# Kernel optimization log

Hardware: AMD Instinct MI355X
Metric: run time of the kernel (lower is better)

## Reference

```python
import math
import jax, jax.numpy as jnp
import numpy as np

ALL_OFFSETS = (1, 2, 3, 4, 5, 6, 7, 8, 9, 11, 13, 15, 16, 23, 32, 64, 128, 256, 512, 1024)
J = len(ALL_OFFSETS)

B, H, N, HD = 2, 16, 8192, 128


def setup_inputs() -> dict:
    key = jax.random.key(0)
    kq, kk, kv, kb, ks = jax.random.split(key, 5)
    return {
        "q": jax.random.normal(kq, (B, H, N, HD), dtype=jnp.float32),
        "k": jax.random.normal(kk, (B, H, N, HD), dtype=jnp.float32),
        "v": jax.random.normal(kv, (B, H, N, HD), dtype=jnp.float32),
        "pos_bias": jax.random.normal(kb, (J, H), dtype=jnp.float32),
        "scale_embed": jax.random.normal(ks, (J, HD), dtype=jnp.float32),
    }


def _dsqg_forward(q, k, v, pos_bias, scale_embed):
    # q,k,v: [B,H,N,HD]; pos_bias: [J,H]; scale_embed: [J,HD]
    b, h, n, hd = q.shape
    sc = 1.0 / math.sqrt(hd)
    idx = jnp.arange(n)
    qf = q.astype(jnp.float32)
    kf = k.astype(jnp.float32)
    vf = v.astype(jnp.float32)
    # learned scale-embedding term fused into scores: (q . se_j) * sc -> [B,H,N,J]
    qse = jnp.einsum('bhnd,jd->bhnj', qf, scale_embed.astype(jnp.float32)) * sc
    pb = pos_bias.astype(jnp.float32)  # [J,H]
    scores = []
    for j, delta in enumerate(ALL_OFFSETS):
        kp = idx - delta
        valid = kp >= 0
        kpc = jnp.clip(kp, 0)
        # gathered-key dot product: one key per query per offset
        s = jnp.einsum('bhnd,bhnd->bhn', qf, kf[:, :, kpc]) * sc
        s = s + pb[j][None, :, None] + qse[..., j]
        s = jnp.where(valid[None, None, :], s, -jnp.inf)
        scores.append(s)
    scores = jnp.stack(scores, axis=-1)  # [B,H,N,J]
    # stable softmax over the J offsets; rows with no valid offset produce 0 output
    m = jnp.max(scores, axis=-1, keepdims=True)
    m_safe = jnp.where(jnp.isfinite(m), m, 0.0)
    e = jnp.where(jnp.isfinite(scores), jnp.exp(scores - m_safe), 0.0)
    l = jnp.sum(e, axis=-1, keepdims=True)
    p = e / jnp.where(l > 0.0, l, 1.0)  # [B,H,N,J]
    out = jnp.zeros_like(qf)
    for j, delta in enumerate(ALL_OFFSETS):
        kpc = jnp.clip(idx - delta, 0)
        out = out + p[..., j:j + 1] * vf[:, :, kpc]
    return out.astype(q.dtype)


def reference(q, k, v, pos_bias, scale_embed):
    return _dsqg_forward(q, k, v, pos_bias, scale_embed)
```

## Files before the change

### kernel.cpp

```cpp
#include <hip/hip_runtime.h>
#include <math.h>

namespace {

constexpr int kB = 2, kH = 16, kN = 8192, kHD = 128, kJ = 20;
constexpr int kTQ = 64;
constexpr float kScale = 0.08838834764831845f;

__global__ __launch_bounds__(256, 4)
void dsqg_fwd(const float* __restrict__ q, const float* __restrict__ k,
              const float* __restrict__ v, const float* __restrict__ pb,
              const float* __restrict__ se, float* __restrict__ out) {
  constexpr int OFFS[kJ] = {1, 2, 3, 4, 5, 6, 7, 8, 9, 11,
                            13, 15, 16, 23, 32, 64, 128, 256, 512, 1024};
  __shared__ float s_se[kJ * kHD];
  __shared__ float s_pb[kJ];

  const int t = threadIdx.x;
  const int bh = blockIdx.y;
  const int h = bh & (kH - 1);
  const int n = blockIdx.x * kTQ + (t >> 2);
  const int part = t & 3;

  for (int i = t; i < kJ * kHD; i += 256) s_se[i] = se[i];
  if (t < kJ) s_pb[t] = pb[t * kH + h];
  __syncthreads();

  const size_t base = (size_t)bh * kN * kHD;
  const float4* qrow = (const float4*)(q + base + (size_t)n * kHD);
  float4 rq[8];
#pragma unroll
  for (int i = 0; i < 8; ++i) rq[i] = qrow[i * 4 + part];

  float sc[kJ];
#pragma unroll
  for (int j = 0; j < kJ; ++j) {
    const int delta = OFFS[j];
    int kr = n - delta;
    kr = kr < 0 ? 0 : kr;
    const float4* krow = (const float4*)(k + base + (size_t)kr * kHD);
    const float4* srow = (const float4*)(s_se + j * kHD);
    float acc = 0.f;
#pragma unroll
    for (int i = 0; i < 8; ++i) {
      float4 kv = krow[i * 4 + part];
      float4 sv = srow[i * 4 + part];
      acc += rq[i].x * (kv.x + sv.x);
      acc += rq[i].y * (kv.y + sv.y);
      acc += rq[i].z * (kv.z + sv.z);
      acc += rq[i].w * (kv.w + sv.w);
    }
    acc += __shfl_xor(acc, 1);
    acc += __shfl_xor(acc, 2);
    const float sj = acc * kScale + s_pb[j];
    sc[j] = (n >= delta) ? sj : -INFINITY;
  }

  float m = -INFINITY;
#pragma unroll
  for (int j = 0; j < kJ; ++j) m = fmaxf(m, sc[j]);
  const float msafe = (m == -INFINITY) ? 0.f : m;
  float l = 0.f;
#pragma unroll
  for (int j = 0; j < kJ; ++j) {
    const float e = (sc[j] == -INFINITY) ? 0.f : __expf(sc[j] - msafe);
    sc[j] = e;
    l += e;
  }
  const float inv = (l > 0.f) ? 1.f / l : 0.f;

  float4 o[8];
#pragma unroll
  for (int i = 0; i < 8; ++i) o[i] = make_float4(0.f, 0.f, 0.f, 0.f);
#pragma unroll
  for (int j = 0; j < kJ; ++j) {
    const float pj = sc[j] * inv;
    int vr = n - OFFS[j];
    vr = vr < 0 ? 0 : vr;
    const float4* vrow = (const float4*)(v + base + (size_t)vr * kHD);
#pragma unroll
    for (int i = 0; i < 8; ++i) {
      float4 vv = vrow[i * 4 + part];
      o[i].x += pj * vv.x;
      o[i].y += pj * vv.y;
      o[i].z += pj * vv.z;
      o[i].w += pj * vv.w;
    }
  }
  float4* orow = (float4*)(out + base + (size_t)n * kHD);
#pragma unroll
  for (int i = 0; i < 8; ++i) orow[i * 4 + part] = o[i];
}

}

extern "C" void kernel_launch(void* const* d_in, const int* in_sizes, int n_in,
                              void* d_out, int out_size, void* d_ws, size_t ws_size,
                              hipStream_t stream) {
  const float* q = (const float*)d_in[0];
  const float* k = (const float*)d_in[1];
  const float* v = (const float*)d_in[2];
  const float* pb = (const float*)d_in[3];
  const float* se = (const float*)d_in[4];
  float* out = (float*)d_out;

  dim3 grid(kN / kTQ, kB * kH);
  dsqg_fwd<<<grid, 256, 0, stream>>>(q, k, v, pb, se, out);
}
```

Before: 760.4 us.

## Swizzle workgroups across XCDs, use nontemporal q/out access, raise occupancy hint

```diff
diff --git a/kernel.cpp b/kernel.cpp
--- a/kernel.cpp
+++ b/kernel.cpp
@@ -5,9 +5,15 @@
 
 constexpr int kB = 2, kH = 16, kN = 8192, kHD = 128, kJ = 20;
 constexpr int kTQ = 64;
+constexpr int kNT = kN / kTQ;
+constexpr int kNWG = kB * kH * kNT;
+constexpr int kNXCD = 8;
+constexpr int kChunk = kNWG / kNXCD;
 constexpr float kScale = 0.08838834764831845f;
 
-__global__ __launch_bounds__(256, 4)
+typedef float f4 __attribute__((ext_vector_type(4)));
+
+__global__ __launch_bounds__(256, 8)
 void dsqg_fwd(const float* __restrict__ q, const float* __restrict__ k,
               const float* __restrict__ v, const float* __restrict__ pb,
               const float* __restrict__ se, float* __restrict__ out) {
@@ -17,9 +23,12 @@
   __shared__ float s_pb[kJ];
 
   const int t = threadIdx.x;
-  const int bh = blockIdx.y;
+  const int lin = blockIdx.x;
+  const int swz = (lin & (kNXCD - 1)) * kChunk + (lin >> 3);
+  const int bh = swz >> 7;
+  const int ntile = swz & (kNT - 1);
   const int h = bh & (kH - 1);
-  const int n = blockIdx.x * kTQ + (t >> 2);
+  const int n = ntile * kTQ + (t >> 2);
   const int part = t & 3;
 
   for (int i = t; i < kJ * kHD; i += 256) s_se[i] = se[i];
@@ -27,10 +36,10 @@
   __syncthreads();
 
   const size_t base = (size_t)bh * kN * kHD;
-  const float4* qrow = (const float4*)(q + base + (size_t)n * kHD);
-  float4 rq[8];
+  const f4* qrow = (const f4*)(q + base + (size_t)n * kHD);
+  f4 rq[8];
 #pragma unroll
-  for (int i = 0; i < 8; ++i) rq[i] = qrow[i * 4 + part];
+  for (int i = 0; i < 8; ++i) rq[i] = __builtin_nontemporal_load(&qrow[i * 4 + part]);
 
   float sc[kJ];
 #pragma unroll
@@ -38,13 +47,13 @@
     const int delta = OFFS[j];
     int kr = n - delta;
     kr = kr < 0 ? 0 : kr;
-    const float4* krow = (const float4*)(k + base + (size_t)kr * kHD);
-    const float4* srow = (const float4*)(s_se + j * kHD);
+    const f4* krow = (const f4*)(k + base + (size_t)kr * kHD);
+    const f4* srow = (const f4*)(s_se + j * kHD);
     float acc = 0.f;
 #pragma unroll
     for (int i = 0; i < 8; ++i) {
-      float4 kv = krow[i * 4 + part];
-      float4 sv = srow[i * 4 + part];
+      f4 kv = krow[i * 4 + part];
+      f4 sv = srow[i * 4 + part];
       acc += rq[i].x * (kv.x + sv.x);
       acc += rq[i].y * (kv.y + sv.y);
       acc += rq[i].z * (kv.z + sv.z);
@@ -69,27 +78,24 @@
   }
   const float inv = (l > 0.f) ? 1.f / l : 0.f;
 
-  float4 o[8];
+  f4 o[8];
 #pragma unroll
-  for (int i = 0; i < 8; ++i) o[i] = make_float4(0.f, 0.f, 0.f, 0.f);
+  for (int i = 0; i < 8; ++i) o[i] = (f4)(0.f);
 #pragma unroll
   for (int j = 0; j < kJ; ++j) {
     const float pj = sc[j] * inv;
     int vr = n - OFFS[j];
     vr = vr < 0 ? 0 : vr;
-    const float4* vrow = (const float4*)(v + base + (size_t)vr * kHD);
+    const f4* vrow = (const f4*)(v + base + (size_t)vr * kHD);
 #pragma unroll
     for (int i = 0; i < 8; ++i) {
-      float4 vv = vrow[i * 4 + part];
-      o[i].x += pj * vv.x;
-      o[i].y += pj * vv.y;
-      o[i].z += pj * vv.z;
-      o[i].w += pj * vv.w;
+      f4 vv = vrow[i * 4 + part];
+      o[i] += pj * vv;
     }
   }
-  float4* orow = (float4*)(out + base + (size_t)n * kHD);
+  f4* orow = (f4*)(out + base + (size_t)n * kHD);
 #pragma unroll
-  for (int i = 0; i < 8; ++i) orow[i * 4 + part] = o[i];
+  for (int i = 0; i < 8; ++i) __builtin_nontemporal_store(o[i], &orow[i * 4 + part]);
 }
 
 }
@@ -104,6 +110,6 @@
   const float* se = (const float*)d_in[4];
   float* out = (float*)d_out;
 
-  dim3 grid(kN / kTQ, kB * kH);
+  dim3 grid(kNWG);
   dsqg_fwd<<<grid, 256, 0, stream>>>(q, k, v, pb, se, out);
 }
```

Measured after the change: 1.718 ms. 126% more time.
